# Kernel tuning notes

Hardware: AMD Instinct MI355X
Metric: run time of the kernel (lower is better)

The kernel has to match this reference:

```python
import jax, jax.numpy as jnp
import numpy as np


def _slice_coeffs(grid, guide):
    """Trilinear slice of bilateral grid at (x, y, guide) per full-res pixel.
    grid:  [B, C, D, Hg, Wg]  (C=12 affine coeffs)
    guide: [B, 1, H, W] in [0, 1]
    returns coeffs [B, C, H, W]
    """
    B, C, D, Hg, Wg = grid.shape
    H, W = guide.shape[2], guide.shape[3]
    g = guide[:, 0]  # [B, H, W]

    # HDRNet sampling convention: pixel centers mapped into grid coords
    gx = (jnp.arange(W, dtype=grid.dtype) + 0.5) / W * Wg - 0.5   # [W]
    gy = (jnp.arange(H, dtype=grid.dtype) + 0.5) / H * Hg - 0.5   # [H]
    gz = g * D - 0.5                                              # [B, H, W]

    gx = jnp.broadcast_to(gx[None, None, :], (B, H, W))
    gy = jnp.broadcast_to(gy[None, :, None], (B, H, W))

    fx0 = jnp.floor(gx); fy0 = jnp.floor(gy); fz0 = jnp.floor(gz)
    wx = gx - fx0; wy = gy - fy0; wz = gz - fz0  # trilinear fractions

    x0 = jnp.clip(fx0.astype(jnp.int32), 0, Wg - 1)
    x1 = jnp.clip(fx0.astype(jnp.int32) + 1, 0, Wg - 1)
    y0 = jnp.clip(fy0.astype(jnp.int32), 0, Hg - 1)
    y1 = jnp.clip(fy0.astype(jnp.int32) + 1, 0, Hg - 1)
    z0 = jnp.clip(fz0.astype(jnp.int32), 0, D - 1)
    z1 = jnp.clip(fz0.astype(jnp.int32) + 1, 0, D - 1)

    def gather_one(gb, zi, yi, xi):
        # gb: [C, D, Hg, Wg]; zi/yi/xi: [H, W] -> [C, H, W]
        return gb[:, zi, yi, xi]

    gather = jax.vmap(gather_one)  # over batch

    out = jnp.zeros((B, C, H, W), dtype=grid.dtype)
    for zi, wzc in ((z0, 1.0 - wz), (z1, wz)):
        for yi, wyc in ((y0, 1.0 - wy), (y1, wy)):
            for xi, wxc in ((x0, 1.0 - wx), (x1, wx)):
                w = (wzc * wyc * wxc)[:, None]  # [B, 1, H, W]
                out = out + w * gather(grid, zi, yi, xi)
    return out


def setup_inputs() -> dict:
    key = jax.random.key(0)
    k1, k2, k3 = jax.random.split(key, 3)
    Bilterial_Grid = jax.random.normal(k1, (4, 12, 8, 16, 16), dtype=jnp.float32)
    Guide = jax.random.uniform(k2, (4, 1, 1024, 1024), dtype=jnp.float32)
    fr = jax.random.uniform(k3, (4, 3, 1024, 1024), dtype=jnp.float32)
    return {"Bilterial_Grid": Bilterial_Grid, "Guide": Guide, "fr": fr}


def reference(Bilterial_Grid, Guide, fr):
    B, _, H, W = fr.shape
    coeffs = _slice_coeffs(Bilterial_Grid, Guide)          # [B, 12, H, W]
    co = coeffs.reshape(B, 3, 4, H, W)                      # 3x4 affine per pixel
    # out_c = sum_i A[c,i] * fr_i + b[c]
    out = jnp.einsum('boihw,bihw->bohw', co[:, :, :3], fr) + co[:, :, 3]
    return out
```

## Files before the change

kernel.cpp:

```cpp
#include <hip/hip_runtime.h>


#define ZSTRIDE 132

using half2v = decltype(__builtin_amdgcn_cvt_pkrtz(0.0f, 0.0f));

static __device__ __forceinline__ half2v pkrtz(float lo, float hi) {
    return __builtin_amdgcn_cvt_pkrtz(lo, hi);
}
static __device__ __forceinline__ half2v u2h2(unsigned int u) {
    return __builtin_bit_cast(half2v, u);
}
static __device__ __forceinline__ unsigned int h2u(half2v h) {
    return __builtin_bit_cast(unsigned int, h);
}

#if __has_builtin(__builtin_amdgcn_fdot2)
#define DOT2(d, wp, acc) __builtin_amdgcn_fdot2(u2h2(d), (wp), (acc), false)
#else
static __device__ __forceinline__ float dot2_sw(unsigned int d, half2v wp, float acc) {
    half2v h = u2h2(d);
    return fmaf((float)wp.x, (float)h.x, fmaf((float)wp.y, (float)h.y, acc));
}
#define DOT2(d, wp, acc) dot2_sw((d), (wp), (acc))
#endif

static __device__ __forceinline__ void corner_dot(
    const unsigned int* __restrict__ cp, half2v wp,
    float& a0, float& a1, float& a2, float& a3)
{
    const uint4 d = *reinterpret_cast<const uint4*>(cp);
    a0 = DOT2(d.x, wp, a0);
    a1 = DOT2(d.y, wp, a1);
    a2 = DOT2(d.z, wp, a2);
    a3 = DOT2(d.w, wp, a3);
}

__global__ __launch_bounds__(256, 3) void slice_apply(
    const float* __restrict__ grid,
    const float* __restrict__ guide,
    const float* __restrict__ fr,
    float* __restrict__ out)
{
    __shared__ __align__(16) unsigned int lds[8 * ZSTRIDE];

    const int b     = blockIdx.y;
    const int tileX = blockIdx.x & 15;
    const int tileY = blockIdx.x >> 4;
    const int t     = threadIdx.x;

    {
        const int py0 = min(max(tileY - 1, 0), 15);
        const int py1 = tileY;
        const int py2 = min(tileY + 1, 15);
        const int px0 = min(max(tileX - 1, 0), 15);
        const int px1 = tileX;
        const int px2 = min(tileX + 1, 15);
        for (int e = t; e < 8 * 9 * 12; e += 256) {
            const int c    = e % 12;
            const int cell = (e / 12) % 9;
            const int s    = e / 108;
            const int s2   = min(s + 1, 7);
            const int gy3  = cell / 3;
            const int gx3  = cell % 3;
            const int ry = (gy3 == 0) ? py0 : ((gy3 == 1) ? py1 : py2);
            const int rx = (gx3 == 0) ? px0 : ((gx3 == 1) ? px1 : px2);
            const int cb = (b * 12 + c) * 8;
            const int sp = ry * 16 + rx;
            const float lo = grid[(cb + s)  * 256 + sp];
            const float hi = grid[(cb + s2) * 256 + sp];
            lds[s * ZSTRIDE + cell * 12 + c] = h2u(pkrtz(lo, hi));
        }
    }
    __syncthreads();

    const int w   = t >> 6;
    const int l   = t & 63;
    const int by  = w >> 1;
    const int bx  = w & 1;
    const int lxq = l & 31;
    const int sub = l >> 5;

    const int xg = tileX * 64 + bx * 32 + lxq;
    const float wx = ((float)(bx * 32 + lxq) + 0.5f) * 0.015625f +
                     (0.5f - (float)bx);
    const float u1 = wx, u0 = 1.0f - wx;

    const int cof0 = ((by + 0) * 3 + (bx + 0)) * 12;
    const int cof1 = ((by + 0) * 3 + (bx + 1)) * 12;
    const int cof2 = ((by + 1) * 3 + (bx + 0)) * 12;
    const int cof3 = ((by + 1) * 3 + (bx + 1)) * 12;

    const int ybase = tileY * 64 + by * 32;

    for (int i = 0; i < 16; ++i) {
        const int ly = by * 32 + i * 2 + sub;
        const int y  = ybase - by * 32 + ly;
        const float wy = ((float)ly + 0.5f) * 0.015625f + (0.5f - (float)by);
        const float v1 = wy, v0 = 1.0f - wy;

        const int gofs = (b * 1024 + y) * 1024 + xg;
        const int fofs = ((b * 3) * 1024 + y) * 1024 + xg;

        const float g  = guide[gofs];
        const float f0 = fr[fofs];
        const float f1 = fr[fofs + 1048576];
        const float f2 = fr[fofs + 2097152];

        const float gz = g * 8.0f - 0.5f;
        int s = (int)floorf(gz);
        s = min(max(s, 0), 7);
        const float wz = fmaxf(gz - (float)s, 0.0f);
        const float zl = 1.0f - wz, zh = wz;
        const unsigned int* sb = &lds[s * ZSTRIDE];

        const float w00 = v0 * u0, w01 = v0 * u1;
        const float w10 = v1 * u0, w11 = v1 * u1;
        const half2v wp0 = pkrtz(w00 * zl, w00 * zh);
        const half2v wp1 = pkrtz(w01 * zl, w01 * zh);
        const half2v wp2 = pkrtz(w10 * zl, w10 * zh);
        const half2v wp3 = pkrtz(w11 * zl, w11 * zh);

        float o0, o1, o2;
        {
            float a0 = 0.f, a1 = 0.f, a2 = 0.f, a3 = 0.f;
            corner_dot(sb + cof0, wp0, a0, a1, a2, a3);
            corner_dot(sb + cof1, wp1, a0, a1, a2, a3);
            corner_dot(sb + cof2, wp2, a0, a1, a2, a3);
            corner_dot(sb + cof3, wp3, a0, a1, a2, a3);
            o0 = fmaf(a0, f0, fmaf(a1, f1, fmaf(a2, f2, a3)));
        }
        {
            float a0 = 0.f, a1 = 0.f, a2 = 0.f, a3 = 0.f;
            corner_dot(sb + cof0 + 4, wp0, a0, a1, a2, a3);
            corner_dot(sb + cof1 + 4, wp1, a0, a1, a2, a3);
            corner_dot(sb + cof2 + 4, wp2, a0, a1, a2, a3);
            corner_dot(sb + cof3 + 4, wp3, a0, a1, a2, a3);
            o1 = fmaf(a0, f0, fmaf(a1, f1, fmaf(a2, f2, a3)));
        }
        {
            float a0 = 0.f, a1 = 0.f, a2 = 0.f, a3 = 0.f;
            corner_dot(sb + cof0 + 8, wp0, a0, a1, a2, a3);
            corner_dot(sb + cof1 + 8, wp1, a0, a1, a2, a3);
            corner_dot(sb + cof2 + 8, wp2, a0, a1, a2, a3);
            corner_dot(sb + cof3 + 8, wp3, a0, a1, a2, a3);
            o2 = fmaf(a0, f0, fmaf(a1, f1, fmaf(a2, f2, a3)));
        }

        out[fofs]           = o0;
        out[fofs + 1048576] = o1;
        out[fofs + 2097152] = o2;
    }
}

extern "C" void kernel_launch(void* const* d_in, const int* in_sizes, int n_in,
                              void* d_out, int out_size, void* d_ws, size_t ws_size,
                              hipStream_t stream) {
    const float* grid  = (const float*)d_in[0];
    const float* guide = (const float*)d_in[1];
    const float* fr    = (const float*)d_in[2];
    float* out = (float*)d_out;

    dim3 g(256, 4);
    dim3 blk(256);
    hipLaunchKernelGGL(slice_apply, g, blk, 0, stream, grid, guide, fr, out);
}
```

Before: 120.1 us.

## Process two pixels per thread with float2 loads and software-prefetched rows

```diff
diff --git a/kernel.cpp b/kernel.cpp
--- a/kernel.cpp
+++ b/kernel.cpp
@@ -36,7 +36,54 @@
     a3 = DOT2(d.w, wp, a3);
 }
 
-__global__ __launch_bounds__(256, 3) void slice_apply(
+static __device__ __forceinline__ void px_eval(
+    const unsigned int* __restrict__ lds,
+    float g, float f0, float f1, float f2,
+    float u0, float u1, float v0, float v1,
+    int cof0, int cof1, int cof2, int cof3,
+    float& o0, float& o1, float& o2)
+{
+    const float gz = g * 8.0f - 0.5f;
+    int s = (int)floorf(gz);
+    s = min(max(s, 0), 7);
+    const float wz = fmaxf(gz - (float)s, 0.0f);
+    const float zl = 1.0f - wz, zh = wz;
+    const unsigned int* sb = &lds[s * ZSTRIDE];
+
+    const float w00 = v0 * u0, w01 = v0 * u1;
+    const float w10 = v1 * u0, w11 = v1 * u1;
+    const half2v wp0 = pkrtz(w00 * zl, w00 * zh);
+    const half2v wp1 = pkrtz(w01 * zl, w01 * zh);
+    const half2v wp2 = pkrtz(w10 * zl, w10 * zh);
+    const half2v wp3 = pkrtz(w11 * zl, w11 * zh);
+
+    {
+        float a0 = 0.f, a1 = 0.f, a2 = 0.f, a3 = 0.f;
+        corner_dot(sb + cof0, wp0, a0, a1, a2, a3);
+        corner_dot(sb + cof1, wp1, a0, a1, a2, a3);
+        corner_dot(sb + cof2, wp2, a0, a1, a2, a3);
+        corner_dot(sb + cof3, wp3, a0, a1, a2, a3);
+        o0 = fmaf(a0, f0, fmaf(a1, f1, fmaf(a2, f2, a3)));
+    }
+    {
+        float a0 = 0.f, a1 = 0.f, a2 = 0.f, a3 = 0.f;
+        corner_dot(sb + cof0 + 4, wp0, a0, a1, a2, a3);
+        corner_dot(sb + cof1 + 4, wp1, a0, a1, a2, a3);
+        corner_dot(sb + cof2 + 4, wp2, a0, a1, a2, a3);
+        corner_dot(sb + cof3 + 4, wp3, a0, a1, a2, a3);
+        o1 = fmaf(a0, f0, fmaf(a1, f1, fmaf(a2, f2, a3)));
+    }
+    {
+        float a0 = 0.f, a1 = 0.f, a2 = 0.f, a3 = 0.f;
+        corner_dot(sb + cof0 + 8, wp0, a0, a1, a2, a3);
+        corner_dot(sb + cof1 + 8, wp1, a0, a1, a2, a3);
+        corner_dot(sb + cof2 + 8, wp2, a0, a1, a2, a3);
+        corner_dot(sb + cof3 + 8, wp3, a0, a1, a2, a3);
+        o2 = fmaf(a0, f0, fmaf(a1, f1, fmaf(a2, f2, a3)));
+    }
+}
+
+__global__ __launch_bounds__(256, 4) void slice_apply(
     const float* __restrict__ grid,
     const float* __restrict__ guide,
     const float* __restrict__ fr,
@@ -78,78 +125,59 @@
     const int l   = t & 63;
     const int by  = w >> 1;
     const int bx  = w & 1;
-    const int lxq = l & 31;
-    const int sub = l >> 5;
+    const int lx2 = l & 15;
+    const int sub = l >> 4;
 
-    const int xg = tileX * 64 + bx * 32 + lxq;
-    const float wx = ((float)(bx * 32 + lxq) + 0.5f) * 0.015625f +
-                     (0.5f - (float)bx);
-    const float u1 = wx, u0 = 1.0f - wx;
+    const int txA = bx * 32 + lx2 * 2;
+    const int xg  = tileX * 64 + txA;
+    const float wxA = ((float)txA + 0.5f) * 0.015625f + (0.5f - (float)bx);
+    const float wxB = wxA + 0.015625f;
+    const float u1A = wxA, u0A = 1.0f - wxA;
+    const float u1B = wxB, u0B = 1.0f - wxB;
 
     const int cof0 = ((by + 0) * 3 + (bx + 0)) * 12;
     const int cof1 = ((by + 0) * 3 + (bx + 1)) * 12;
     const int cof2 = ((by + 1) * 3 + (bx + 0)) * 12;
     const int cof3 = ((by + 1) * 3 + (bx + 1)) * 12;
 
-    const int ybase = tileY * 64 + by * 32;
+    const int y0   = tileY * 64 + by * 32 + sub;
+    int gofs = (b * 1024 + y0) * 1024 + xg;
+    int fofs = ((b * 3) * 1024 + y0) * 1024 + xg;
 
-    for (int i = 0; i < 16; ++i) {
-        const int ly = by * 32 + i * 2 + sub;
-        const int y  = ybase - by * 32 + ly;
+    float2 gv  = *reinterpret_cast<const float2*>(guide + gofs);
+    float2 f0v = *reinterpret_cast<const float2*>(fr + fofs);
+    float2 f1v = *reinterpret_cast<const float2*>(fr + fofs + 1048576);
+    float2 f2v = *reinterpret_cast<const float2*>(fr + fofs + 2097152);
+
+    #pragma unroll
+    for (int i = 0; i < 8; ++i) {
+        float2 gn = gv, f0n = f0v, f1n = f1v, f2n = f2v;
+        if (i < 7) {
+            const int gofs_n = gofs + 4 * 1024;
+            const int fofs_n = fofs + 4 * 1024;
+            gn  = *reinterpret_cast<const float2*>(guide + gofs_n);
+            f0n = *reinterpret_cast<const float2*>(fr + fofs_n);
+            f1n = *reinterpret_cast<const float2*>(fr + fofs_n + 1048576);
+            f2n = *reinterpret_cast<const float2*>(fr + fofs_n + 2097152);
+        }
+
+        const int ly = by * 32 + i * 4 + sub;
         const float wy = ((float)ly + 0.5f) * 0.015625f + (0.5f - (float)by);
         const float v1 = wy, v0 = 1.0f - wy;
 
-        const int gofs = (b * 1024 + y) * 1024 + xg;
-        const int fofs = ((b * 3) * 1024 + y) * 1024 + xg;
+        float oA0, oA1, oA2, oB0, oB1, oB2;
+        px_eval(lds, gv.x, f0v.x, f1v.x, f2v.x, u0A, u1A, v0, v1,
+                cof0, cof1, cof2, cof3, oA0, oA1, oA2);
+        px_eval(lds, gv.y, f0v.y, f1v.y, f2v.y, u0B, u1B, v0, v1,
+                cof0, cof1, cof2, cof3, oB0, oB1, oB2);
 
-        const float g  = guide[gofs];
-        const float f0 = fr[fofs];
-        const float f1 = fr[fofs + 1048576];
-        const float f2 = fr[fofs + 2097152];
+        *reinterpret_cast<float2*>(out + fofs)           = make_float2(oA0, oB0);
+        *reinterpret_cast<float2*>(out + fofs + 1048576) = make_float2(oA1, oB1);
+        *reinterpret_cast<float2*>(out + fofs + 2097152) = make_float2(oA2, oB2);
 
-        const float gz = g * 8.0f - 0.5f;
-        int s = (int)floorf(gz);
-        s = min(max(s, 0), 7);
-        const float wz = fmaxf(gz - (float)s, 0.0f);
-        const float zl = 1.0f - wz, zh = wz;
-        const unsigned int* sb = &lds[s * ZSTRIDE];
-
-        const float w00 = v0 * u0, w01 = v0 * u1;
-        const float w10 = v1 * u0, w11 = v1 * u1;
-        const half2v wp0 = pkrtz(w00 * zl, w00 * zh);
-        const half2v wp1 = pkrtz(w01 * zl, w01 * zh);
-        const half2v wp2 = pkrtz(w10 * zl, w10 * zh);
-        const half2v wp3 = pkrtz(w11 * zl, w11 * zh);
-
-        float o0, o1, o2;
-        {
-            float a0 = 0.f, a1 = 0.f, a2 = 0.f, a3 = 0.f;
-            corner_dot(sb + cof0, wp0, a0, a1, a2, a3);
-            corner_dot(sb + cof1, wp1, a0, a1, a2, a3);
-            corner_dot(sb + cof2, wp2, a0, a1, a2, a3);
-            corner_dot(sb + cof3, wp3, a0, a1, a2, a3);
-            o0 = fmaf(a0, f0, fmaf(a1, f1, fmaf(a2, f2, a3)));
-        }
-        {
-            float a0 = 0.f, a1 = 0.f, a2 = 0.f, a3 = 0.f;
-            corner_dot(sb + cof0 + 4, wp0, a0, a1, a2, a3);
-            corner_dot(sb + cof1 + 4, wp1, a0, a1, a2, a3);
-            corner_dot(sb + cof2 + 4, wp2, a0, a1, a2, a3);
-            corner_dot(sb + cof3 + 4, wp3, a0, a1, a2, a3);
-            o1 = fmaf(a0, f0, fmaf(a1, f1, fmaf(a2, f2, a3)));
-        }
-        {
-            float a0 = 0.f, a1 = 0.f, a2 = 0.f, a3 = 0.f;
-            corner_dot(sb + cof0 + 8, wp0, a0, a1, a2, a3);
-            corner_dot(sb + cof1 + 8, wp1, a0, a1, a2, a3);
-            corner_dot(sb + cof2 + 8, wp2, a0, a1, a2, a3);
-            corner_dot(sb + cof3 + 8, wp3, a0, a1, a2, a3);
-            o2 = fmaf(a0, f0, fmaf(a1, f1, fmaf(a2, f2, a3)));
-        }
-
-        out[fofs]           = o0;
-        out[fofs + 1048576] = o1;
-        out[fofs + 2097152] = o2;
+        gofs += 4 * 1024;
+        fofs += 4 * 1024;
+        gv = gn; f0v = f0n; f1v = f1n; f2v = f2n;
     }
 }
 
```

New measurement: 117.5 us, median of 2. 2.2% less time.
